# Performance work log

Measured on AMD Instinct MI355X. Metric: run time of the kernel, lower is better.

The kernel has to match this reference:

```python
import jax, jax.numpy as jnp
import numpy as np

B, S, D, H = 4, 2048, 512, 8
HD = D // H


def setup_inputs() -> dict:
    key = jax.random.key(0)
    ks = jax.random.split(key, 12)
    x = jax.random.normal(ks[0], (B, S, D), dtype=jnp.float32)
    docking_scores = jax.random.uniform(ks[1], (B, S), dtype=jnp.float32)
    mask = jax.random.randint(ks[2], (B, S), 0, 2).astype(jnp.bool_)
    s = 0.02
    Wq = jax.random.normal(ks[3], (D, D), dtype=jnp.float32) * s
    bq = jnp.zeros((D,), dtype=jnp.float32)
    Wk = jax.random.normal(ks[4], (D, D), dtype=jnp.float32) * s
    bk = jnp.zeros((D,), dtype=jnp.float32)
    Wv = jax.random.normal(ks[5], (D, D), dtype=jnp.float32) * s
    bv = jnp.zeros((D,), dtype=jnp.float32)
    Wo = jax.random.normal(ks[6], (D, D), dtype=jnp.float32) * s
    bo = jnp.zeros((D,), dtype=jnp.float32)
    alpha = jnp.float32(0.5)
    beta = jnp.float32(0.5)
    return {"x": x, "docking_scores": docking_scores, "mask": mask,
            "Wq": Wq, "bq": bq, "Wk": Wk, "bk": bk, "Wv": Wv, "bv": bv,
            "Wo": Wo, "bo": bo, "alpha": alpha, "beta": beta}


def reference(x, docking_scores, mask, Wq, bq, Wk, bk, Wv, bv, Wo, bo, alpha, beta):
    # daa_type == ATTENTION: attention + docking-score blend (alpha unused here).
    b, s, d = x.shape
    # zero docking scores at padded positions; shape (B, S, 1)
    ds = jnp.where(mask[..., None], docking_scores[..., None], 0.0)
    def proj(W, bias):
        return (jnp.einsum('bsd,ed->bse', x, W) + bias).reshape(b, s, H, HD).transpose(0, 2, 1, 3)
    Q = proj(Wq, bq)  # (B, H, S, HD)
    K = proj(Wk, bk)
    V = proj(Wv, bv)
    scores = jnp.einsum('bhqd,bhkd->bhqk', Q, K) / jnp.sqrt(jnp.float32(HD))
    scores = jnp.where(mask[:, None, None, :], scores, -jnp.inf)  # key-padding mask
    attn = jax.nn.softmax(scores, axis=-1)  # (B, H, S, S)
    # docking blend: (B,1,S,1) broadcasts over heads and key dim (faithful to torch expand)
    attn = (1.0 - beta) * attn + beta * ds[:, None, :, :]
    ctx = jnp.einsum('bhqk,bhkd->bhqd', attn, V)
    ctx = ctx.transpose(0, 2, 1, 3).reshape(b, s, d)
    return jnp.einsum('bsd,od->bso', ctx, Wo) + bo
```

## Files before the change

### kernel.cpp

```cpp
#include <hip/hip_runtime.h>
#include <hip/hip_bf16.h>

#define B_ 4
#define S_ 2048
#define D_ 512
#define H_ 8
#define HD_ 64

typedef unsigned int uint;
typedef unsigned short ushort_t;
typedef __attribute__((ext_vector_type(4))) float f32x4;
typedef __attribute__((ext_vector_type(16))) float f32x16;
typedef __attribute__((ext_vector_type(8))) short bf16x8;

#if __has_builtin(__builtin_amdgcn_exp2f)
#define EXP2F __builtin_amdgcn_exp2f
#else
#define EXP2F exp2f
#endif

__device__ __forceinline__ float bf2f(unsigned short u){ union{uint i;float f;}c; c.i = (uint)u<<16; return c.f; }
__device__ __forceinline__ unsigned short f2bf(float f){
    __hip_bfloat16 h = __float2bfloat16(f);
    return *reinterpret_cast<unsigned short*>(&h);
}

__device__ __forceinline__ void gload16(const unsigned short* g, const ushort_t* l){
    __builtin_amdgcn_global_load_lds(
        (const __attribute__((address_space(1))) unsigned int*)g,
        (__attribute__((address_space(3))) unsigned int*)l, 16, 0, 0);
}

__global__ __launch_bounds__(256) void convert_all(
    const float* __restrict__ x,
    const float* __restrict__ Wq, const float* __restrict__ Wk,
    const float* __restrict__ Wv, const float* __restrict__ Wo,
    const int* __restrict__ mask,
    ushort_t* __restrict__ xb, ushort_t* __restrict__ Wqkvb, ushort_t* __restrict__ Wob,
    float* __restrict__ mbg)
{
    const int NX = 1048576;
    const int NW = 65536;
    const int total = NX + 4 * NW;
    for (int i = blockIdx.x * 256 + threadIdx.x; i < total; i += gridDim.x * 256) {
        const float* src; ushort_t* dst; int so, dofs;
        if (i < NX) { src = x; so = i; dst = xb; dofs = i; }
        else if (i < NX + 3 * NW) {
            int j = i - NX;
            if (j < NW)          { src = Wq; so = j; }
            else if (j < 2 * NW) { src = Wk; so = j - NW; }
            else                 { src = Wv; so = j - 2 * NW; }
            dst = Wqkvb; dofs = j;
        } else { int k = i - NX - 3 * NW; src = Wo; so = k; dst = Wob; dofs = k; }
        float4 v = ((const float4*)src)[so];
        ushort4 u;
        u.x = f2bf(v.x); u.y = f2bf(v.y); u.z = f2bf(v.z); u.w = f2bf(v.w);
        ((ushort4*)dst)[dofs] = u;
    }
    for (int i = blockIdx.x * 256 + threadIdx.x; i < 2048; i += gridDim.x * 256) {
        int4 mv = ((const int4*)mask)[i];
        float4 o;
        o.x = mv.x ? 0.f : -1e30f;
        o.y = mv.y ? 0.f : -1e30f;
        o.z = mv.z ? 0.f : -1e30f;
        o.w = mv.w ? 0.f : -1e30f;
        ((float4*)mbg)[i] = o;
    }
}

template<int MODE>
__global__ __launch_bounds__(256) void gemm_mfma(
    const ushort_t* __restrict__ A, const ushort_t* __restrict__ Bw,
    const float* __restrict__ b0, const float* __restrict__ b1, const float* __restrict__ b2,
    ushort_t* __restrict__ O0, ushort_t* __restrict__ O1, ushort_t* __restrict__ O2,
    float* __restrict__ Of)
{
    __shared__ __align__(16) unsigned char smem[34816];
    ushort_t* sA = (ushort_t*)smem;
    ushort_t* sB = sA + 8192;

    const int t = threadIdx.x, w = t >> 6, l = t & 63, g = l >> 4, c = l & 15;
    const int wm = w >> 1, wn = w & 1;
    const int row0 = blockIdx.y * 128, col0 = blockIdx.x * 128;

    const ushort_t* aSrc[4]; const ushort_t* bSrc[4];
    ushort_t* aDst[4]; ushort_t* bDst[4];
    #pragma unroll
    for (int i = 0; i < 4; ++i) {
        int cc = i * 256 + t;
        int row = cc >> 3, slot = (cc & 7) ^ (row & 7);
        aSrc[i] = A  + (size_t)(row0 + row) * 512 + slot * 8;
        bSrc[i] = Bw + (size_t)(col0 + row) * 512 + slot * 8;
        aDst[i] = sA + (i * 256 + w * 64) * 8;
        bDst[i] = sB + (i * 256 + w * 64) * 8;
    }

    f32x4 acc[4][4];
    #pragma unroll
    for (int mi = 0; mi < 4; ++mi)
        #pragma unroll
        for (int ni = 0; ni < 4; ++ni) acc[mi][ni] = (f32x4)0.f;

    for (int ks = 0; ks < 8; ++ks) {
        #pragma unroll
        for (int i = 0; i < 4; ++i) {
            gload16(aSrc[i], aDst[i]);
            gload16(bSrc[i], bDst[i]);
        }
        __syncthreads();
        #pragma unroll
        for (int kh = 0; kh < 2; ++kh) {
            bf16x8 af[4], bfv[4];
            const int sw = (((kh << 2) | g) ^ (c & 7)) << 3;
            #pragma unroll
            for (int mi = 0; mi < 4; ++mi)
                af[mi] = *(const bf16x8*)&sA[(wm * 64 + mi * 16 + c) * 64 + sw];
            #pragma unroll
            for (int ni = 0; ni < 4; ++ni)
                bfv[ni] = *(const bf16x8*)&sB[(wn * 64 + ni * 16 + c) * 64 + sw];
            #pragma unroll
            for (int mi = 0; mi < 4; ++mi)
                #pragma unroll
                for (int ni = 0; ni < 4; ++ni)
                    acc[mi][ni] = __builtin_amdgcn_mfma_f32_16x16x32_bf16(af[mi], bfv[ni], acc[mi][ni], 0, 0, 0);
        }
        #pragma unroll
        for (int i = 0; i < 4; ++i) { aSrc[i] += 64; bSrc[i] += 64; }
        __syncthreads();
    }

    if (MODE == 1) {
        #pragma unroll
        for (int mi = 0; mi < 4; ++mi)
            #pragma unroll
            for (int ni = 0; ni < 4; ++ni) {
                int n = col0 + wn * 64 + ni * 16 + c;
                float bias = b0[n];
                #pragma unroll
                for (int r = 0; r < 4; ++r)
                    Of[(size_t)(row0 + wm * 64 + mi * 16 + 4 * g + r) * 512 + n] =
                        acc[mi][ni][r] + bias;
            }
    } else {
        const int which = col0 >> 9;
        const float* bias = which == 0 ? b0 : (which == 1 ? b1 : b2);
        ushort_t (*Cl)[136] = (ushort_t(*)[136])smem;
        if (which < 2) {
            #pragma unroll
            for (int mi = 0; mi < 4; ++mi)
                #pragma unroll
                for (int ni = 0; ni < 4; ++ni) {
                    int n = wn * 64 + ni * 16 + c;
                    float bb = bias[(col0 & 511) + n];
                    #pragma unroll
                    for (int r = 0; r < 4; ++r)
                        Cl[wm * 64 + mi * 16 + 4 * g + r][n] = f2bf(acc[mi][ni][r] + bb);
                }
        } else {
            #pragma unroll
            for (int mi = 0; mi < 4; ++mi)
                #pragma unroll
                for (int ni = 0; ni < 4; ++ni) {
                    int n = wn * 64 + ni * 16 + c;
                    float bb = bias[(col0 & 511) + n];
                    #pragma unroll
                    for (int r = 0; r < 4; ++r)
                        Cl[n][wm * 64 + mi * 16 + 4 * g + r] = f2bf(acc[mi][ni][r] + bb);
                }
        }
        __syncthreads();
        const int r = t >> 1, half = t & 1;
        const int b = row0 >> 11;
        if (which < 2) {
            ushort_t* Out = which == 0 ? O0 : O1;
            int s = (row0 & 2047) + r;
            int e = (col0 & 511) + half * 64;
            int h = e >> 6;
            ushort_t* dst = Out + (((size_t)(b * 8 + h) * 2048 + s) << 6);
            #pragma unroll
            for (int j = 0; j < 8; ++j)
                *(bf16x8*)(dst + j * 8) = *(const bf16x8*)&Cl[r][half * 64 + j * 8];
        } else {
            int e = (col0 & 511) + r;
            int h = e >> 6, d = e & 63;
            int s0 = (row0 & 2047) + half * 64;
            ushort_t* dst = O2 + ((size_t)(b * 8 + h) * 64 + d) * 2048 + s0;
            #pragma unroll
            for (int j = 0; j < 8; ++j)
                *(bf16x8*)(dst + j * 8) = *(const bf16x8*)&Cl[r][half * 64 + j * 8];
        }
    }
}

__global__ __launch_bounds__(256) void vsum2(
    const __hip_bfloat16* __restrict__ Vt, float* __restrict__ Vsum)
{
    const int row = blockIdx.x * 4 + (threadIdx.x >> 6);
    const int l = threadIdx.x & 63;
    const unsigned short* p = (const unsigned short*)Vt + (size_t)row * S_;
    float s = 0.f;
    #pragma unroll
    for (int i = 0; i < 4; ++i) {
        uint4 u = *(const uint4*)(p + i * 512 + l * 8);
        s += bf2f((unsigned short)(u.x & 0xffff)) + bf2f((unsigned short)(u.x >> 16));
        s += bf2f((unsigned short)(u.y & 0xffff)) + bf2f((unsigned short)(u.y >> 16));
        s += bf2f((unsigned short)(u.z & 0xffff)) + bf2f((unsigned short)(u.z >> 16));
        s += bf2f((unsigned short)(u.w & 0xffff)) + bf2f((unsigned short)(u.w >> 16));
    }
    #pragma unroll
    for (int m = 1; m < 64; m <<= 1) s += __shfl_xor(s, m);
    if (l == 0) Vsum[row] = s;
}

__global__ __launch_bounds__(256, 2) void attn_mfma(
    const __hip_bfloat16* __restrict__ Qb, const __hip_bfloat16* __restrict__ Kb,
    const __hip_bfloat16* __restrict__ Vt, const float* __restrict__ Vsum,
    const float* __restrict__ dock, const int* __restrict__ mask,
    const float* __restrict__ mbg, const float* __restrict__ beta_p,
    ushort_t* __restrict__ ctxb)
{
    __shared__ __align__(16) unsigned char smem[32768];
    ushort_t* Kbuf = (ushort_t*)smem;
    ushort_t* Vbuf = (ushort_t*)(smem + 16384);

    const int flat = blockIdx.x;
    const int xcd = flat & 7, idx = flat >> 3;
    const int bh = ((idx >> 4) << 3) | xcd;
    const int qtile = idx & 15;
    const int b = bh >> 3, h8 = bh & 7;
    const int t = threadIdx.x, w = t >> 6, lam = t & 63;
    const int lq = lam & 31, hf = lam >> 5;
    const int q0 = qtile * 128 + w * 32;
    const int qg = q0 + lq;
    const float beta = beta_p[0];
    const ushort_t* Kp = (const ushort_t*)Kb + (size_t)bh * S_ * HD_;
    const ushort_t* Vp = (const ushort_t*)Vt + (size_t)bh * HD_ * S_;
    const float* mbp = mbg + b * S_;

    const int srow = t >> 2, squad = t & 3;
    const int sx = ((srow & 7) << 1) | ((srow >> 3) & 1);
    int wof[4];
    #pragma unroll
    for (int i = 0; i < 4; ++i)
        wof[i] = srow * 64 + ((((squad << 2) | i) ^ sx) << 2);

    const int xr = ((lq & 7) << 1) | ((lq >> 3) & 1);

    bf16x8 qf[4];
    #pragma unroll
    for (int hd = 0; hd < 4; ++hd)
        qf[hd] = *(const bf16x8*)((const ushort_t*)Qb +
            ((size_t)bh * S_ + qg) * HD_ + hd * 16 + hf * 8);

    f32x16 cacc[2];
    cacc[0] = (f32x16)0.f;
    cacc[1] = (f32x16)0.f;
    float l_ = 0.f;
    const float CSC = 0.18033688011112042f;

    {
        uint4 kg0 = *(const uint4*)(Kp + (size_t)srow * 64 + squad * 16);
        uint4 kg1 = *(const uint4*)(Kp + (size_t)srow * 64 + squad * 16 + 8);
        uint4 vg0 = *(const uint4*)(Vp + (size_t)srow * 2048 + squad * 16);
        uint4 vg1 = *(const uint4*)(Vp + (size_t)srow * 2048 + squad * 16 + 8);
        *(uint2*)(Kbuf + wof[0]) = make_uint2(kg0.x, kg0.y);
        *(uint2*)(Kbuf + wof[1]) = make_uint2(kg0.z, kg0.w);
        *(uint2*)(Kbuf + wof[2]) = make_uint2(kg1.x, kg1.y);
        *(uint2*)(Kbuf + wof[3]) = make_uint2(kg1.z, kg1.w);
        *(uint2*)(Vbuf + wof[0]) = make_uint2(vg0.x, vg0.y);
        *(uint2*)(Vbuf + wof[1]) = make_uint2(vg0.z, vg0.w);
        *(uint2*)(Vbuf + wof[2]) = make_uint2(vg1.x, vg1.y);
        *(uint2*)(Vbuf + wof[3]) = make_uint2(vg1.z, vg1.w);
    }
    __syncthreads();

    for (int k0 = 0; k0 < S_; k0 += 64) {
        const int par = (k0 >> 6) & 1;
        const ushort_t* KBp = Kbuf + par * 4096;
        const ushort_t* VBp = Vbuf + par * 4096;
        const bool pre = (k0 + 64 < S_);

        uint4 kg0, kg1, vg0, vg1;
        if (pre) {
            kg0 = *(const uint4*)(Kp + (size_t)(k0 + 64 + srow) * 64 + squad * 16);
            kg1 = *(const uint4*)(Kp + (size_t)(k0 + 64 + srow) * 64 + squad * 16 + 8);
            vg0 = *(const uint4*)(Vp + (size_t)srow * 2048 + k0 + 64 + squad * 16);
            vg1 = *(const uint4*)(Vp + (size_t)srow * 2048 + k0 + 64 + squad * 16 + 8);
        }
        float4 mb[2][4];
        #pragma unroll
        for (int kt2 = 0; kt2 < 2; ++kt2)
            #pragma unroll
            for (int qd = 0; qd < 4; ++qd)
                mb[kt2][qd] = *(const float4*)(mbp + k0 + kt2 * 32 + qd * 8 + hf * 4);

        f32x16 sacc[2];
        sacc[0] = (f32x16)0.f;
        sacc[1] = (f32x16)0.f;
        __builtin_amdgcn_s_setprio(1);
        #pragma unroll
        for (int kt2 = 0; kt2 < 2; ++kt2) {
            const ushort_t* kr = KBp + (kt2 * 32 + lq) * 64;
            #pragma unroll
            for (int hd = 0; hd < 4; ++hd) {
                uint2 lo = *(const uint2*)(kr + ((((hd << 2) | (hf << 1)) ^ xr) << 2));
                uint2 hi = *(const uint2*)(kr + ((((hd << 2) | (hf << 1) | 1) ^ xr) << 2));
                union { bf16x8 v; uint4 u; } kf;
                kf.u = make_uint4(lo.x, lo.y, hi.x, hi.y);
                sacc[kt2] = __builtin_amdgcn_mfma_f32_32x32x16_bf16(kf.v, qf[hd], sacc[kt2], 0, 0, 0);
            }
        }
        __builtin_amdgcn_s_setprio(0);

        float p[2][16];
        float ps = 0.f;
        #pragma unroll
        for (int kt2 = 0; kt2 < 2; ++kt2)
            #pragma unroll
            for (int qd = 0; qd < 4; ++qd) {
                float4 m4 = mb[kt2][qd];
                float p0 = EXP2F(fmaf(sacc[kt2][qd * 4 + 0], CSC, m4.x));
                float p1 = EXP2F(fmaf(sacc[kt2][qd * 4 + 1], CSC, m4.y));
                float p2 = EXP2F(fmaf(sacc[kt2][qd * 4 + 2], CSC, m4.z));
                float p3 = EXP2F(fmaf(sacc[kt2][qd * 4 + 3], CSC, m4.w));
                p[kt2][qd * 4 + 0] = p0; p[kt2][qd * 4 + 1] = p1;
                p[kt2][qd * 4 + 2] = p2; p[kt2][qd * 4 + 3] = p3;
                ps += p0 + p1 + p2 + p3;
            }
        l_ += ps;

        __builtin_amdgcn_s_setprio(1);
        #pragma unroll
        for (int kt2 = 0; kt2 < 2; ++kt2)
            #pragma unroll
            for (int ks = 0; ks < 2; ++ks) {
                bf16x8 pf;
                #pragma unroll
                for (int m = 0; m < 8; ++m)
                    pf[m] = (short)f2bf(p[kt2][ks * 8 + m]);
                #pragma unroll
                for (int dt = 0; dt < 2; ++dt) {
                    const ushort_t* vr = VBp + (dt * 32 + lq) * 64;
                    uint2 lo = *(const uint2*)(vr + (((8 * kt2 + 4 * ks + hf) ^ xr) << 2));
                    uint2 hi = *(const uint2*)(vr + (((8 * kt2 + 4 * ks + 2 + hf) ^ xr) << 2));
                    union { bf16x8 v; uint4 u; } vf;
                    vf.u = make_uint4(lo.x, lo.y, hi.x, hi.y);
                    cacc[dt] = __builtin_amdgcn_mfma_f32_32x32x16_bf16(vf.v, pf, cacc[dt], 0, 0, 0);
                }
            }
        __builtin_amdgcn_s_setprio(0);

        if (pre) {
            ushort_t* KD = Kbuf + (par ^ 1) * 4096;
            ushort_t* VD = Vbuf + (par ^ 1) * 4096;
            *(uint2*)(KD + wof[0]) = make_uint2(kg0.x, kg0.y);
            *(uint2*)(KD + wof[1]) = make_uint2(kg0.z, kg0.w);
            *(uint2*)(KD + wof[2]) = make_uint2(kg1.x, kg1.y);
            *(uint2*)(KD + wof[3]) = make_uint2(kg1.z, kg1.w);
            *(uint2*)(VD + wof[0]) = make_uint2(vg0.x, vg0.y);
            *(uint2*)(VD + wof[1]) = make_uint2(vg0.z, vg0.w);
            *(uint2*)(VD + wof[2]) = make_uint2(vg1.x, vg1.y);
            *(uint2*)(VD + wof[3]) = make_uint2(vg1.z, vg1.w);
        }
        __syncthreads();
    }

    l_ += __shfl_xor(l_, 32);

    __syncthreads();

    ushort_t* ctxl = (ushort_t*)smem;
    {
        const float w1 = (1.f - beta) / l_;
        const float dq = (mask[b * S_ + qg] ? dock[b * S_ + qg] : 0.f) * beta;
        #pragma unroll
        for (int dt = 0; dt < 2; ++dt)
            #pragma unroll
            for (int qd = 0; qd < 4; ++qd) {
                const int d0 = dt * 32 + qd * 8 + hf * 4;
                float4 vs = *(const float4*)(Vsum + bh * 64 + d0);
                float o0 = cacc[dt][qd * 4 + 0] * w1 + dq * vs.x;
                float o1 = cacc[dt][qd * 4 + 1] * w1 + dq * vs.y;
                float o2 = cacc[dt][qd * 4 + 2] * w1 + dq * vs.z;
                float o3 = cacc[dt][qd * 4 + 3] * w1 + dq * vs.w;
                uint lo = (uint)f2bf(o0) | ((uint)f2bf(o1) << 16);
                uint hi = (uint)f2bf(o2) | ((uint)f2bf(o3) << 16);
                *(uint2*)(ctxl + (size_t)w * 2304 + lq * 72 + d0) = make_uint2(lo, hi);
            }
    }
    __syncthreads();
    {
        const int qloc = lam >> 1, half = lam & 1;
        ushort_t* cp = ctxb + ((size_t)(b * 2048 + q0 + qloc)) * 512 + h8 * 64 + half * 32;
        const ushort_t* rp = ctxl + (size_t)w * 2304 + qloc * 72 + half * 32;
        #pragma unroll
        for (int j = 0; j < 4; ++j)
            *(bf16x8*)(cp + j * 8) = *(const bf16x8*)(rp + j * 8);
    }
}

extern "C" void kernel_launch(void* const* d_in, const int* in_sizes, int n_in,
                              void* d_out, int out_size, void* d_ws, size_t ws_size,
                              hipStream_t stream)
{
    const float* x    = (const float*)d_in[0];
    const float* dock = (const float*)d_in[1];
    const int*   mask = (const int*)d_in[2];
    const float* Wq   = (const float*)d_in[3];
    const float* bq   = (const float*)d_in[4];
    const float* Wk   = (const float*)d_in[5];
    const float* bk   = (const float*)d_in[6];
    const float* Wv   = (const float*)d_in[7];
    const float* bv   = (const float*)d_in[8];
    const float* Wo   = (const float*)d_in[9];
    const float* bo   = (const float*)d_in[10];
    const float* beta = (const float*)d_in[12];
    float* out = (float*)d_out;

    const size_t nqkv = (size_t)B_ * H_ * S_ * HD_;
    ushort_t* xb    = (ushort_t*)d_ws;
    ushort_t* Qb    = xb + nqkv;
    ushort_t* Kb    = Qb + nqkv;
    ushort_t* Vt    = Kb + nqkv;
    ushort_t* Wqkvb = Vt + nqkv;
    ushort_t* Wob   = Wqkvb + 1536 * 512;
    float*    Vsum  = (float*)(Wob + 512 * 512);
    float*    mbg   = Vsum + 2048;
    ushort_t* ctxb  = xb;

    convert_all<<<1280, 256, 0, stream>>>(x, Wq, Wk, Wv, Wo, mask, xb, Wqkvb, Wob, mbg);
    gemm_mfma<0><<<dim3(12, 64), 256, 0, stream>>>(xb, Wqkvb, bq, bk, bv, Qb, Kb, Vt, nullptr);
    vsum2<<<512, 256, 0, stream>>>((const __hip_bfloat16*)Vt, Vsum);
    attn_mfma<<<512, 256, 0, stream>>>(
        (const __hip_bfloat16*)Qb, (const __hip_bfloat16*)Kb, (const __hip_bfloat16*)Vt,
        Vsum, dock, mask, mbg, beta, ctxb);
    gemm_mfma<1><<<dim3(4, 64), 256, 0, stream>>>(ctxb, Wob, bo, nullptr, nullptr,
                                                  nullptr, nullptr, nullptr, out);
}
```

Measured before the change: 108.4 us.

## Software-pipeline attention: compute next tile's QK^T while doing current softmax and PV

Restructures the key loop into a three-buffer rotating LDS ring for K and V. The QK^T MFMAs for the next tile are issued before the softmax exponentials and PV MFMAs of the current tile, and global prefetch now runs two tiles ahead. The goal is to overlap the exp/VALU work with matrix-core work and hide load latency. In exchange LDS grows from 32KB to 48KB and a second score accumulator adds register pressure, which may reduce occupancy at 2 blocks per CU.

```diff
diff --git a/kernel.cpp b/kernel.cpp
--- a/kernel.cpp
+++ b/kernel.cpp
@@ -219,9 +219,7 @@
     const float* __restrict__ mbg, const float* __restrict__ beta_p,
     ushort_t* __restrict__ ctxb)
 {
-    __shared__ __align__(16) unsigned char smem[32768];
-    ushort_t* Kbuf = (ushort_t*)smem;
-    ushort_t* Vbuf = (ushort_t*)(smem + 16384);
+    __shared__ __align__(16) unsigned char smem[49152];
 
     const int flat = blockIdx.x;
     const int xcd = flat & 7, idx = flat >> 3;
@@ -237,6 +235,13 @@
     const ushort_t* Vp = (const ushort_t*)Vt + (size_t)bh * HD_ * S_;
     const float* mbp = mbg + b * S_;
 
+    ushort_t* Kc = (ushort_t*)smem;
+    ushort_t* Kn = (ushort_t*)(smem + 8192);
+    ushort_t* Ks = (ushort_t*)(smem + 16384);
+    ushort_t* Vc = (ushort_t*)(smem + 24576);
+    ushort_t* Vn = (ushort_t*)(smem + 32768);
+    ushort_t* Vs = (ushort_t*)(smem + 40960);
+
     const int srow = t >> 2, squad = t & 3;
     const int sx = ((srow & 7) << 1) | ((srow >> 3) & 1);
     int wof[4];
@@ -258,112 +263,141 @@
     float l_ = 0.f;
     const float CSC = 0.18033688011112042f;
 
+#define COMMIT(DST, G0, G1) do {                                               \
+    *(uint2*)((DST) + wof[0]) = make_uint2((G0).x, (G0).y);                    \
+    *(uint2*)((DST) + wof[1]) = make_uint2((G0).z, (G0).w);                    \
+    *(uint2*)((DST) + wof[2]) = make_uint2((G1).x, (G1).y);                    \
+    *(uint2*)((DST) + wof[3]) = make_uint2((G1).z, (G1).w);                    \
+} while (0)
+
     {
-        uint4 kg0 = *(const uint4*)(Kp + (size_t)srow * 64 + squad * 16);
-        uint4 kg1 = *(const uint4*)(Kp + (size_t)srow * 64 + squad * 16 + 8);
-        uint4 vg0 = *(const uint4*)(Vp + (size_t)srow * 2048 + squad * 16);
-        uint4 vg1 = *(const uint4*)(Vp + (size_t)srow * 2048 + squad * 16 + 8);
-        *(uint2*)(Kbuf + wof[0]) = make_uint2(kg0.x, kg0.y);
-        *(uint2*)(Kbuf + wof[1]) = make_uint2(kg0.z, kg0.w);
-        *(uint2*)(Kbuf + wof[2]) = make_uint2(kg1.x, kg1.y);
-        *(uint2*)(Kbuf + wof[3]) = make_uint2(kg1.z, kg1.w);
-        *(uint2*)(Vbuf + wof[0]) = make_uint2(vg0.x, vg0.y);
-        *(uint2*)(Vbuf + wof[1]) = make_uint2(vg0.z, vg0.w);
-        *(uint2*)(Vbuf + wof[2]) = make_uint2(vg1.x, vg1.y);
-        *(uint2*)(Vbuf + wof[3]) = make_uint2(vg1.z, vg1.w);
+        uint4 a0 = *(const uint4*)(Kp + (size_t)srow * 64 + squad * 16);
+        uint4 a1 = *(const uint4*)(Kp + (size_t)srow * 64 + squad * 16 + 8);
+        uint4 b0 = *(const uint4*)(Vp + (size_t)srow * 2048 + squad * 16);
+        uint4 b1 = *(const uint4*)(Vp + (size_t)srow * 2048 + squad * 16 + 8);
+        uint4 c0 = *(const uint4*)(Kp + (size_t)(64 + srow) * 64 + squad * 16);
+        uint4 c1 = *(const uint4*)(Kp + (size_t)(64 + srow) * 64 + squad * 16 + 8);
+        uint4 d0 = *(const uint4*)(Vp + (size_t)srow * 2048 + 64 + squad * 16);
+        uint4 d1 = *(const uint4*)(Vp + (size_t)srow * 2048 + 64 + squad * 16 + 8);
+        COMMIT(Kc, a0, a1);
+        COMMIT(Vc, b0, b1);
+        COMMIT(Kn, c0, c1);
+        COMMIT(Vn, d0, d1);
     }
     __syncthreads();
 
-    for (int k0 = 0; k0 < S_; k0 += 64) {
-        const int par = (k0 >> 6) & 1;
-        const ushort_t* KBp = Kbuf + par * 4096;
-        const ushort_t* VBp = Vbuf + par * 4096;
-        const bool pre = (k0 + 64 < S_);
-
-        uint4 kg0, kg1, vg0, vg1;
-        if (pre) {
-            kg0 = *(const uint4*)(Kp + (size_t)(k0 + 64 + srow) * 64 + squad * 16);
-            kg1 = *(const uint4*)(Kp + (size_t)(k0 + 64 + srow) * 64 + squad * 16 + 8);
-            vg0 = *(const uint4*)(Vp + (size_t)srow * 2048 + k0 + 64 + squad * 16);
-            vg1 = *(const uint4*)(Vp + (size_t)srow * 2048 + k0 + 64 + squad * 16 + 8);
-        }
-        float4 mb[2][4];
-        #pragma unroll
-        for (int kt2 = 0; kt2 < 2; ++kt2)
-            #pragma unroll
-            for (int qd = 0; qd < 4; ++qd)
-                mb[kt2][qd] = *(const float4*)(mbp + k0 + kt2 * 32 + qd * 8 + hf * 4);
-
-        f32x16 sacc[2];
-        sacc[0] = (f32x16)0.f;
-        sacc[1] = (f32x16)0.f;
+    f32x16 saccA[2], saccB[2];
+
+    {
+        saccA[0] = (f32x16)0.f;
+        saccA[1] = (f32x16)0.f;
         __builtin_amdgcn_s_setprio(1);
         #pragma unroll
         for (int kt2 = 0; kt2 < 2; ++kt2) {
-            const ushort_t* kr = KBp + (kt2 * 32 + lq) * 64;
+            const ushort_t* kr = Kc + (kt2 * 32 + lq) * 64;
             #pragma unroll
             for (int hd = 0; hd < 4; ++hd) {
                 uint2 lo = *(const uint2*)(kr + ((((hd << 2) | (hf << 1)) ^ xr) << 2));
                 uint2 hi = *(const uint2*)(kr + ((((hd << 2) | (hf << 1) | 1) ^ xr) << 2));
                 union { bf16x8 v; uint4 u; } kf;
                 kf.u = make_uint4(lo.x, lo.y, hi.x, hi.y);
-                sacc[kt2] = __builtin_amdgcn_mfma_f32_32x32x16_bf16(kf.v, qf[hd], sacc[kt2], 0, 0, 0);
+                saccA[kt2] = __builtin_amdgcn_mfma_f32_32x32x16_bf16(kf.v, qf[hd], saccA[kt2], 0, 0, 0);
             }
         }
         __builtin_amdgcn_s_setprio(0);
-
-        float p[2][16];
-        float ps = 0.f;
-        #pragma unroll
-        for (int kt2 = 0; kt2 < 2; ++kt2)
-            #pragma unroll
-            for (int qd = 0; qd < 4; ++qd) {
-                float4 m4 = mb[kt2][qd];
-                float p0 = EXP2F(fmaf(sacc[kt2][qd * 4 + 0], CSC, m4.x));
-                float p1 = EXP2F(fmaf(sacc[kt2][qd * 4 + 1], CSC, m4.y));
-                float p2 = EXP2F(fmaf(sacc[kt2][qd * 4 + 2], CSC, m4.z));
-                float p3 = EXP2F(fmaf(sacc[kt2][qd * 4 + 3], CSC, m4.w));
-                p[kt2][qd * 4 + 0] = p0; p[kt2][qd * 4 + 1] = p1;
-                p[kt2][qd * 4 + 2] = p2; p[kt2][qd * 4 + 3] = p3;
-                ps += p0 + p1 + p2 + p3;
-            }
-        l_ += ps;
-
-        __builtin_amdgcn_s_setprio(1);
-        #pragma unroll
-        for (int kt2 = 0; kt2 < 2; ++kt2)
-            #pragma unroll
-            for (int ks = 0; ks < 2; ++ks) {
-                bf16x8 pf;
-                #pragma unroll
-                for (int m = 0; m < 8; ++m)
-                    pf[m] = (short)f2bf(p[kt2][ks * 8 + m]);
-                #pragma unroll
-                for (int dt = 0; dt < 2; ++dt) {
-                    const ushort_t* vr = VBp + (dt * 32 + lq) * 64;
-                    uint2 lo = *(const uint2*)(vr + (((8 * kt2 + 4 * ks + hf) ^ xr) << 2));
-                    uint2 hi = *(const uint2*)(vr + (((8 * kt2 + 4 * ks + 2 + hf) ^ xr) << 2));
-                    union { bf16x8 v; uint4 u; } vf;
-                    vf.u = make_uint4(lo.x, lo.y, hi.x, hi.y);
-                    cacc[dt] = __builtin_amdgcn_mfma_f32_32x32x16_bf16(vf.v, pf, cacc[dt], 0, 0, 0);
-                }
-            }
-        __builtin_amdgcn_s_setprio(0);
-
-        if (pre) {
-            ushort_t* KD = Kbuf + (par ^ 1) * 4096;
-            ushort_t* VD = Vbuf + (par ^ 1) * 4096;
-            *(uint2*)(KD + wof[0]) = make_uint2(kg0.x, kg0.y);
-            *(uint2*)(KD + wof[1]) = make_uint2(kg0.z, kg0.w);
-            *(uint2*)(KD + wof[2]) = make_uint2(kg1.x, kg1.y);
-            *(uint2*)(KD + wof[3]) = make_uint2(kg1.z, kg1.w);
-            *(uint2*)(VD + wof[0]) = make_uint2(vg0.x, vg0.y);
-            *(uint2*)(VD + wof[1]) = make_uint2(vg0.z, vg0.w);
-            *(uint2*)(VD + wof[2]) = make_uint2(vg1.x, vg1.y);
-            *(uint2*)(VD + wof[3]) = make_uint2(vg1.z, vg1.w);
-        }
-        __syncthreads();
-    }
+    }
+
+#define BODY(K, SC, SN) do {                                                   \
+    const int k0_ = (K) * 64;                                                  \
+    const bool pre_ = (K) + 2 < 32;                                            \
+          \
+    uint4 kg0, kg1, vg0, vg1;                                                  \
+    if (pre_) {                                                                \
+        const int kn_ = k0_ + 128;                                             \
+        kg0 = *(const uint4*)(Kp + (size_t)(kn_ + srow) * 64 + squad * 16);    \
+        kg1 = *(const uint4*)(Kp + (size_t)(kn_ + srow) * 64 + squad * 16 + 8);\
+        vg0 = *(const uint4*)(Vp + (size_t)srow * 2048 + kn_ + squad * 16);    \
+        vg1 = *(const uint4*)(Vp + (size_t)srow * 2048 + kn_ + squad * 16 + 8);\
+    }                                                                          \
+               \
+    if ((K) + 1 < 32) {                                                        \
+        SN[0] = (f32x16)0.f;                                                   \
+        SN[1] = (f32x16)0.f;                                                   \
+        __builtin_amdgcn_s_setprio(1);                                         \
+        _Pragma("unroll")                                                      \
+        for (int kt2 = 0; kt2 < 2; ++kt2) {                                    \
+            const ushort_t* kr = Kn + (kt2 * 32 + lq) * 64;                    \
+            _Pragma("unroll")                                                  \
+            for (int hd = 0; hd < 4; ++hd) {                                   \
+                uint2 lo = *(const uint2*)(kr + ((((hd << 2) | (hf << 1)) ^ xr) << 2));      \
+                uint2 hi = *(const uint2*)(kr + ((((hd << 2) | (hf << 1) | 1) ^ xr) << 2));  \
+                union { bf16x8 v; uint4 u; } kf;                               \
+                kf.u = make_uint4(lo.x, lo.y, hi.x, hi.y);                     \
+                SN[kt2] = __builtin_amdgcn_mfma_f32_32x32x16_bf16(kf.v, qf[hd], SN[kt2], 0, 0, 0); \
+            }                                                                  \
+        }                                                                      \
+        __builtin_amdgcn_s_setprio(0);                                         \
+    }                                                                          \
+                    \
+    float p[2][16];                                                            \
+    float ps = 0.f;                                                            \
+    _Pragma("unroll")                                                          \
+    for (int kt2 = 0; kt2 < 2; ++kt2)                                          \
+        _Pragma("unroll")                                                      \
+        for (int qd = 0; qd < 4; ++qd) {                                       \
+            float4 m4 = *(const float4*)(mbp + k0_ + kt2 * 32 + qd * 8 + hf * 4); \
+            float p0 = EXP2F(fmaf(SC[kt2][qd * 4 + 0], CSC, m4.x));            \
+            float p1 = EXP2F(fmaf(SC[kt2][qd * 4 + 1], CSC, m4.y));            \
+            float p2 = EXP2F(fmaf(SC[kt2][qd * 4 + 2], CSC, m4.z));            \
+            float p3 = EXP2F(fmaf(SC[kt2][qd * 4 + 3], CSC, m4.w));            \
+            p[kt2][qd * 4 + 0] = p0; p[kt2][qd * 4 + 1] = p1;                  \
+            p[kt2][qd * 4 + 2] = p2; p[kt2][qd * 4 + 3] = p3;                  \
+            ps += p0 + p1 + p2 + p3;                                           \
+        }                                                                      \
+    l_ += ps;                                                                  \
+        \
+    __builtin_amdgcn_s_setprio(1);                                             \
+    _Pragma("unroll")                                                          \
+    for (int kt2 = 0; kt2 < 2; ++kt2)                                          \
+        _Pragma("unroll")                                                      \
+        for (int ks = 0; ks < 2; ++ks) {                                       \
+            bf16x8 pf;                                                         \
+            _Pragma("unroll")                                                  \
+            for (int m = 0; m < 8; ++m)                                        \
+                pf[m] = (short)f2bf(p[kt2][ks * 8 + m]);                       \
+            _Pragma("unroll")                                                  \
+            for (int dt = 0; dt < 2; ++dt) {                                   \
+                const ushort_t* vr = Vc + (dt * 32 + lq) * 64;                 \
+                uint2 lo = *(const uint2*)(vr + (((8 * kt2 + 4 * ks + hf) ^ xr) << 2));      \
+                uint2 hi = *(const uint2*)(vr + (((8 * kt2 + 4 * ks + 2 + hf) ^ xr) << 2));  \
+                union { bf16x8 v; uint4 u; } vf;                               \
+                vf.u = make_uint4(lo.x, lo.y, hi.x, hi.y);                     \
+                cacc[dt] = __builtin_amdgcn_mfma_f32_32x32x16_bf16(vf.v, pf, cacc[dt], 0, 0, 0); \
+            }                                                                  \
+        }                                                                      \
+    __builtin_amdgcn_s_setprio(0);                                             \
+     \
+    if (pre_) {                                                                \
+        COMMIT(Ks, kg0, kg1);                                                  \
+        COMMIT(Vs, vg0, vg1);                                                  \
+    }                                                                          \
+    __syncthreads();                                                           \
+} while (0)
+
+#define ROT() do {                                                             \
+    ushort_t* tmp_ = Kc; Kc = Kn; Kn = Ks; Ks = tmp_;                          \
+    tmp_ = Vc; Vc = Vn; Vn = Vs; Vs = tmp_;                                    \
+} while (0)
+
+    for (int k = 0; k < 32; k += 2) {
+        BODY(k, saccA, saccB);
+        ROT();
+        BODY(k + 1, saccB, saccA);
+        ROT();
+    }
+#undef BODY
+#undef ROT
+#undef COMMIT
 
     l_ += __shfl_xor(l_, 32);
 
```

Measured after the change: 111.0 us. +2.4%, slower.

## Split attention key range across two wave groups per block and combine via LDS

Applied to the files above, without the earlier changes.

The attention block grows from 4 to 8 waves. Each pair of waves shares a query tile, and each half processes half of the key sequence with its own double-buffered K/V staging in a 64KB LDS allocation. The second half writes its partial context and row sums to LDS, and the first half adds them before normalising and writing out. This halves the serial key loop per wave to raise parallelism and latency hiding, at the cost of more LDS per block (lower block occupancy) and an extra reduction step.

```diff
diff --git a/kernel.cpp b/kernel.cpp
--- a/kernel.cpp
+++ b/kernel.cpp
@@ -212,16 +212,14 @@
     if (l == 0) Vsum[row] = s;
 }
 
-__global__ __launch_bounds__(256, 2) void attn_mfma(
+__global__ __launch_bounds__(512, 4) void attn_mfma(
     const __hip_bfloat16* __restrict__ Qb, const __hip_bfloat16* __restrict__ Kb,
     const __hip_bfloat16* __restrict__ Vt, const float* __restrict__ Vsum,
     const float* __restrict__ dock, const int* __restrict__ mask,
     const float* __restrict__ mbg, const float* __restrict__ beta_p,
     ushort_t* __restrict__ ctxb)
 {
-    __shared__ __align__(16) unsigned char smem[32768];
-    ushort_t* Kbuf = (ushort_t*)smem;
-    ushort_t* Vbuf = (ushort_t*)(smem + 16384);
+    __shared__ __align__(16) unsigned char smem[65536];
 
     const int flat = blockIdx.x;
     const int xcd = flat & 7, idx = flat >> 3;
@@ -229,15 +227,22 @@
     const int qtile = idx & 15;
     const int b = bh >> 3, h8 = bh & 7;
     const int t = threadIdx.x, w = t >> 6, lam = t & 63;
+    const int qsub = w & 3, half = w >> 2;
     const int lq = lam & 31, hf = lam >> 5;
-    const int q0 = qtile * 128 + w * 32;
+    const int q0 = qtile * 128 + qsub * 32;
     const int qg = q0 + lq;
     const float beta = beta_p[0];
     const ushort_t* Kp = (const ushort_t*)Kb + (size_t)bh * S_ * HD_;
     const ushort_t* Vp = (const ushort_t*)Vt + (size_t)bh * HD_ * S_;
-    const float* mbp = mbg + b * S_;
-
-    const int srow = t >> 2, squad = t & 3;
+    const ushort_t* Kh = Kp + (size_t)half * 1024 * 64;
+    const ushort_t* Vh = Vp + half * 1024;
+    const float* mbph = mbg + b * S_ + half * 1024;
+
+    ushort_t* Kbuf = (ushort_t*)smem + half * 8192;
+    ushort_t* Vbuf = (ushort_t*)(smem + 32768) + half * 8192;
+
+    const int tl = t & 255;
+    const int srow = tl >> 2, squad = tl & 3;
     const int sx = ((srow & 7) << 1) | ((srow >> 3) & 1);
     int wof[4];
     #pragma unroll
@@ -259,10 +264,10 @@
     const float CSC = 0.18033688011112042f;
 
     {
-        uint4 kg0 = *(const uint4*)(Kp + (size_t)srow * 64 + squad * 16);
-        uint4 kg1 = *(const uint4*)(Kp + (size_t)srow * 64 + squad * 16 + 8);
-        uint4 vg0 = *(const uint4*)(Vp + (size_t)srow * 2048 + squad * 16);
-        uint4 vg1 = *(const uint4*)(Vp + (size_t)srow * 2048 + squad * 16 + 8);
+        uint4 kg0 = *(const uint4*)(Kh + (size_t)srow * 64 + squad * 16);
+        uint4 kg1 = *(const uint4*)(Kh + (size_t)srow * 64 + squad * 16 + 8);
+        uint4 vg0 = *(const uint4*)(Vh + (size_t)srow * 2048 + squad * 16);
+        uint4 vg1 = *(const uint4*)(Vh + (size_t)srow * 2048 + squad * 16 + 8);
         *(uint2*)(Kbuf + wof[0]) = make_uint2(kg0.x, kg0.y);
         *(uint2*)(Kbuf + wof[1]) = make_uint2(kg0.z, kg0.w);
         *(uint2*)(Kbuf + wof[2]) = make_uint2(kg1.x, kg1.y);
@@ -274,25 +279,25 @@
     }
     __syncthreads();
 
-    for (int k0 = 0; k0 < S_; k0 += 64) {
+    for (int k0 = 0; k0 < 1024; k0 += 64) {
         const int par = (k0 >> 6) & 1;
         const ushort_t* KBp = Kbuf + par * 4096;
         const ushort_t* VBp = Vbuf + par * 4096;
-        const bool pre = (k0 + 64 < S_);
+        const bool pre = (k0 + 64 < 1024);
 
         uint4 kg0, kg1, vg0, vg1;
         if (pre) {
-            kg0 = *(const uint4*)(Kp + (size_t)(k0 + 64 + srow) * 64 + squad * 16);
-            kg1 = *(const uint4*)(Kp + (size_t)(k0 + 64 + srow) * 64 + squad * 16 + 8);
-            vg0 = *(const uint4*)(Vp + (size_t)srow * 2048 + k0 + 64 + squad * 16);
-            vg1 = *(const uint4*)(Vp + (size_t)srow * 2048 + k0 + 64 + squad * 16 + 8);
+            kg0 = *(const uint4*)(Kh + (size_t)(k0 + 64 + srow) * 64 + squad * 16);
+            kg1 = *(const uint4*)(Kh + (size_t)(k0 + 64 + srow) * 64 + squad * 16 + 8);
+            vg0 = *(const uint4*)(Vh + (size_t)srow * 2048 + k0 + 64 + squad * 16);
+            vg1 = *(const uint4*)(Vh + (size_t)srow * 2048 + k0 + 64 + squad * 16 + 8);
         }
         float4 mb[2][4];
         #pragma unroll
         for (int kt2 = 0; kt2 < 2; ++kt2)
             #pragma unroll
             for (int qd = 0; qd < 4; ++qd)
-                mb[kt2][qd] = *(const float4*)(mbp + k0 + kt2 * 32 + qd * 8 + hf * 4);
+                mb[kt2][qd] = *(const float4*)(mbph + k0 + kt2 * 32 + qd * 8 + hf * 4);
 
         f32x16 sacc[2];
         sacc[0] = (f32x16)0.f;
@@ -369,8 +374,28 @@
 
     __syncthreads();
 
-    ushort_t* ctxl = (ushort_t*)smem;
-    {
+    float* combO = (float*)smem;
+    float* combL = (float*)(smem + 32768);
+    ushort_t* ctxl = (ushort_t*)(smem + 33280);
+
+    if (half == 1) {
+        #pragma unroll
+        for (int dt = 0; dt < 2; ++dt)
+            #pragma unroll
+            for (int qd = 0; qd < 4; ++qd) {
+                const int d0 = dt * 32 + qd * 8 + hf * 4;
+                float4 v;
+                v.x = cacc[dt][qd * 4 + 0];
+                v.y = cacc[dt][qd * 4 + 1];
+                v.z = cacc[dt][qd * 4 + 2];
+                v.w = cacc[dt][qd * 4 + 3];
+                *(float4*)&combO[((size_t)qsub * 32 + lq) * 64 + d0] = v;
+            }
+        if (hf == 0) combL[qsub * 32 + lq] = l_;
+    }
+    __syncthreads();
+    if (half == 0) {
+        l_ += combL[qsub * 32 + lq];
         const float w1 = (1.f - beta) / l_;
         const float dq = (mask[b * S_ + qg] ? dock[b * S_ + qg] : 0.f) * beta;
         #pragma unroll
@@ -378,21 +403,22 @@
             #pragma unroll
             for (int qd = 0; qd < 4; ++qd) {
                 const int d0 = dt * 32 + qd * 8 + hf * 4;
+                float4 po = *(const float4*)&combO[((size_t)qsub * 32 + lq) * 64 + d0];
                 float4 vs = *(const float4*)(Vsum + bh * 64 + d0);
-                float o0 = cacc[dt][qd * 4 + 0] * w1 + dq * vs.x;
-                float o1 = cacc[dt][qd * 4 + 1] * w1 + dq * vs.y;
-                float o2 = cacc[dt][qd * 4 + 2] * w1 + dq * vs.z;
-                float o3 = cacc[dt][qd * 4 + 3] * w1 + dq * vs.w;
+                float o0 = (cacc[dt][qd * 4 + 0] + po.x) * w1 + dq * vs.x;
+                float o1 = (cacc[dt][qd * 4 + 1] + po.y) * w1 + dq * vs.y;
+                float o2 = (cacc[dt][qd * 4 + 2] + po.z) * w1 + dq * vs.z;
+                float o3 = (cacc[dt][qd * 4 + 3] + po.w) * w1 + dq * vs.w;
                 uint lo = (uint)f2bf(o0) | ((uint)f2bf(o1) << 16);
                 uint hi = (uint)f2bf(o2) | ((uint)f2bf(o3) << 16);
-                *(uint2*)(ctxl + (size_t)w * 2304 + lq * 72 + d0) = make_uint2(lo, hi);
+                *(uint2*)(ctxl + (size_t)qsub * 2304 + lq * 72 + d0) = make_uint2(lo, hi);
             }
     }
     __syncthreads();
-    {
-        const int qloc = lam >> 1, half = lam & 1;
-        ushort_t* cp = ctxb + ((size_t)(b * 2048 + q0 + qloc)) * 512 + h8 * 64 + half * 32;
-        const ushort_t* rp = ctxl + (size_t)w * 2304 + qloc * 72 + half * 32;
+    if (half == 0) {
+        const int qloc = lam >> 1, hl = lam & 1;
+        ushort_t* cp = ctxb + ((size_t)(b * 2048 + q0 + qloc)) * 512 + h8 * 64 + hl * 32;
+        const ushort_t* rp = ctxl + (size_t)qsub * 2304 + qloc * 72 + hl * 32;
         #pragma unroll
         for (int j = 0; j < 4; ++j)
             *(bf16x8*)(cp + j * 8) = *(const bf16x8*)(rp + j * 8);
@@ -431,7 +457,7 @@
     convert_all<<<1280, 256, 0, stream>>>(x, Wq, Wk, Wv, Wo, mask, xb, Wqkvb, Wob, mbg);
     gemm_mfma<0><<<dim3(12, 64), 256, 0, stream>>>(xb, Wqkvb, bq, bk, bv, Qb, Kb, Vt, nullptr);
     vsum2<<<512, 256, 0, stream>>>((const __hip_bfloat16*)Vt, Vsum);
-    attn_mfma<<<512, 256, 0, stream>>>(
+    attn_mfma<<<512, 512, 0, stream>>>(
         (const __hip_bfloat16*)Qb, (const __hip_bfloat16*)Kb, (const __hip_bfloat16*)Vt,
         Vsum, dock, mask, mbg, beta, ctxb);
     gemm_mfma<1><<<dim3(4, 64), 256, 0, stream>>>(ctxb, Wob, bo, nullptr, nullptr,
```

Result: slower. 405.1 us (+273.7%).

## Fuse V column-sum into QKV GEMM epilogue and remap GEMM grid per XCD

Applied to the files above, without the earlier changes.

Removes the separate vsum2 kernel. The V-transpose epilogue of the QKV GEMM now accumulates each row's bf16 sum and adds it into Vsum with an atomic, after a memset clears Vsum. Both GEMMs also switch to a 1D grid that gives each XCD a contiguous band of row tiles, aiming for better L2 reuse of the A rows. The cost is an extra memset, some atomics, and float-sum ordering that is no longer deterministic.

```diff
diff --git a/kernel.cpp b/kernel.cpp
--- a/kernel.cpp
+++ b/kernel.cpp
@@ -73,7 +73,7 @@
     const ushort_t* __restrict__ A, const ushort_t* __restrict__ Bw,
     const float* __restrict__ b0, const float* __restrict__ b1, const float* __restrict__ b2,
     ushort_t* __restrict__ O0, ushort_t* __restrict__ O1, ushort_t* __restrict__ O2,
-    float* __restrict__ Of)
+    float* __restrict__ Of, float* __restrict__ Vsum)
 {
     __shared__ __align__(16) unsigned char smem[34816];
     ushort_t* sA = (ushort_t*)smem;
@@ -81,7 +81,13 @@
 
     const int t = threadIdx.x, w = t >> 6, l = t & 63, g = l >> 4, c = l & 15;
     const int wm = w >> 1, wn = w & 1;
-    const int row0 = blockIdx.y * 128, col0 = blockIdx.x * 128;
+
+    const int flat = blockIdx.x;
+    const int xcd = flat & 7, j0 = flat >> 3;
+    const int NC = (MODE == 0) ? 12 : 4;
+    const int rowt = xcd * 8 + j0 / NC;
+    const int colt = j0 % NC;
+    const int row0 = rowt * 128, col0 = colt * 128;
 
     const ushort_t* aSrc[4]; const ushort_t* bSrc[4];
     ushort_t* aDst[4]; ushort_t* bDst[4];
@@ -178,38 +184,25 @@
             int h = e >> 6;
             ushort_t* dst = Out + (((size_t)(b * 8 + h) * 2048 + s) << 6);
             #pragma unroll
-            for (int j = 0; j < 8; ++j)
-                *(bf16x8*)(dst + j * 8) = *(const bf16x8*)&Cl[r][half * 64 + j * 8];
+            for (int j2 = 0; j2 < 8; ++j2)
+                *(bf16x8*)(dst + j2 * 8) = *(const bf16x8*)&Cl[r][half * 64 + j2 * 8];
         } else {
             int e = (col0 & 511) + r;
             int h = e >> 6, d = e & 63;
             int s0 = (row0 & 2047) + half * 64;
             ushort_t* dst = O2 + ((size_t)(b * 8 + h) * 64 + d) * 2048 + s0;
-            #pragma unroll
-            for (int j = 0; j < 8; ++j)
-                *(bf16x8*)(dst + j * 8) = *(const bf16x8*)&Cl[r][half * 64 + j * 8];
-        }
-    }
-}
-
-__global__ __launch_bounds__(256) void vsum2(
-    const __hip_bfloat16* __restrict__ Vt, float* __restrict__ Vsum)
-{
-    const int row = blockIdx.x * 4 + (threadIdx.x >> 6);
-    const int l = threadIdx.x & 63;
-    const unsigned short* p = (const unsigned short*)Vt + (size_t)row * S_;
-    float s = 0.f;
-    #pragma unroll
-    for (int i = 0; i < 4; ++i) {
-        uint4 u = *(const uint4*)(p + i * 512 + l * 8);
-        s += bf2f((unsigned short)(u.x & 0xffff)) + bf2f((unsigned short)(u.x >> 16));
-        s += bf2f((unsigned short)(u.y & 0xffff)) + bf2f((unsigned short)(u.y >> 16));
-        s += bf2f((unsigned short)(u.z & 0xffff)) + bf2f((unsigned short)(u.z >> 16));
-        s += bf2f((unsigned short)(u.w & 0xffff)) + bf2f((unsigned short)(u.w >> 16));
-    }
-    #pragma unroll
-    for (int m = 1; m < 64; m <<= 1) s += __shfl_xor(s, m);
-    if (l == 0) Vsum[row] = s;
+            float vs_ = 0.f;
+            #pragma unroll
+            for (int j2 = 0; j2 < 8; ++j2) {
+                bf16x8 v = *(const bf16x8*)&Cl[r][half * 64 + j2 * 8];
+                *(bf16x8*)(dst + j2 * 8) = v;
+                #pragma unroll
+                for (int e2 = 0; e2 < 8; ++e2)
+                    vs_ += bf2f((unsigned short)v[e2]);
+            }
+            atomicAdd(&Vsum[(b * 8 + h) * 64 + d], vs_);
+        }
+    }
 }
 
 __global__ __launch_bounds__(256, 2) void attn_mfma(
@@ -428,12 +421,12 @@
     float*    mbg   = Vsum + 2048;
     ushort_t* ctxb  = xb;
 
+    hipMemsetAsync(Vsum, 0, 2048 * sizeof(float), stream);
     convert_all<<<1280, 256, 0, stream>>>(x, Wq, Wk, Wv, Wo, mask, xb, Wqkvb, Wob, mbg);
-    gemm_mfma<0><<<dim3(12, 64), 256, 0, stream>>>(xb, Wqkvb, bq, bk, bv, Qb, Kb, Vt, nullptr);
-    vsum2<<<512, 256, 0, stream>>>((const __hip_bfloat16*)Vt, Vsum);
+    gemm_mfma<0><<<768, 256, 0, stream>>>(xb, Wqkvb, bq, bk, bv, Qb, Kb, Vt, nullptr, Vsum);
     attn_mfma<<<512, 256, 0, stream>>>(
         (const __hip_bfloat16*)Qb, (const __hip_bfloat16*)Kb, (const __hip_bfloat16*)Vt,
         Vsum, dock, mask, mbg, beta, ctxb);
-    gemm_mfma<1><<<dim3(4, 64), 256, 0, stream>>>(ctxb, Wob, bo, nullptr, nullptr,
-                                                  nullptr, nullptr, nullptr, out);
-}
+    gemm_mfma<1><<<256, 256, 0, stream>>>(ctxb, Wob, bo, nullptr, nullptr,
+                                          nullptr, nullptr, nullptr, out, nullptr);
+}
```

Measured after the change: 111.5 us. +2.9%, slower.
